# Kernel optimization log

Measured on AMD Instinct MI355X. Metric: run time of the kernel, lower is better.

Reference implementation:

```python
import jax, jax.numpy as jnp
import numpy as np
import math

B, L, D, H, TOPK = 2, 2048, 1024, 16, 5
DK = D // H
U = min(TOPK * int(np.ceil(np.log1p(L))), L)  # = 40 selected queries


def setup_inputs() -> dict:
    k = jax.random.key(0)
    ks = jax.random.split(k, 9)
    s = 1.0 / math.sqrt(D)  # ~ torch Linear init scale
    return {
        "query": jax.random.normal(ks[0], (B, L, D), jnp.float32),
        "key": jax.random.normal(ks[1], (B, L, D), jnp.float32),
        "value": jax.random.normal(ks[2], (B, L, D), jnp.float32),
        "Wq": jax.random.uniform(ks[3], (D, D), jnp.float32, -s, s),
        "bq": jax.random.uniform(ks[4], (D,), jnp.float32, -s, s),
        "Wk": jax.random.uniform(ks[5], (D, D), jnp.float32, -s, s),
        "bk": jax.random.uniform(ks[6], (D,), jnp.float32, -s, s),
        "Wv": jax.random.uniform(ks[7], (D, D), jnp.float32, -s, s),
        "bv": jax.random.uniform(ks[8], (D,), jnp.float32, -s, s),
    }


def reference(query, key, value, Wq, bq, Wk, bk, Wv, bv):
    # torch Linear: y = x @ W.T + b ; split_heads -> [B, H, L, DK]
    def split(x):
        return x.reshape(B, L, H, DK).transpose(0, 2, 1, 3)

    Q = split(query @ Wq.T + bq)
    K = split(key @ Wk.T + bk)
    V = split(value @ Wv.T + bv)

    # Full score matrix [B,H,L,L]; used only for the sparsity measure M
    # (original's Q_K_sample actually uses full K; sampling is dead code).
    scores_full = jnp.einsum('bhqd,bhkd->bhqk', Q, K)
    M = scores_full.max(axis=-1) - scores_full.mean(axis=-1)  # [B,H,L]

    _, M_top = jax.lax.top_k(M, U)  # [B,H,U] (torch uses sorted=False; set identical)

    Q_red = jnp.take_along_axis(Q, M_top[..., None], axis=2)  # [B,H,U,DK]
    attn_scores = jnp.einsum('bhqd,bhkd->bhqk', Q_red, K) / math.sqrt(DK)

    # default causal mask rows gathered at the selected query positions
    causal = jnp.triu(jnp.ones((L, L), jnp.float32), 1)  # [L_Q, L_K]
    attn_scores = attn_scores + causal[M_top] * (-1e9)   # [B,H,U,L]

    attn_probs = jax.nn.softmax(attn_scores, axis=-1)
    attn = jnp.einsum('bhql,bhld->bqhd', attn_probs, V).reshape(B, U, D)
    return attn, attn_probs
```

## Files before the change

### kernel.cpp

```cpp
#include <hip/hip_runtime.h>
#include <hip/hip_bf16.h>

#define BB 2
#define LL 2048
#define DD 1024
#define HH 16
#define DK 64
#define UU 40
#define BH (BB*HH)

typedef unsigned short u16;
typedef float f32x4 __attribute__((ext_vector_type(4)));
typedef short s16x8 __attribute__((ext_vector_type(8)));

__device__ inline float b2f_r8(u16 x) {
    union { unsigned short u; __hip_bfloat16 b; } c; c.u = x;
    return __bfloat162float(c.b);
}
__device__ inline float ldf_r8(const void* p, size_t i, int isF) {
    return isF ? ((const float*)p)[i] : b2f_r8(((const u16*)p)[i]);
}
__device__ inline f32x4 ld4_r8(const void* p, size_t i, int isF) {
    if (isF) return *(const f32x4*)((const float*)p + i);
    ushort4 v = *(const ushort4*)((const u16*)p + i);
    f32x4 r;
    r[0] = b2f_r8(v.x); r[1] = b2f_r8(v.y); r[2] = b2f_r8(v.z); r[3] = b2f_r8(v.w);
    return r;
}
__device__ inline void cvt2_r8(float x, u16& h, u16& l) {
    union { __hip_bfloat16 b; u16 u; } ch, cl;
    ch.b = __float2bfloat16(x);
    float hf = __bfloat162float(ch.b);
    cl.b = __float2bfloat16(x - hf);
    h = ch.u; l = cl.u;
}

__global__ __launch_bounds__(256) void detect_dtype_r8(const u16* __restrict__ q,
                                                       int* __restrict__ flag) {
    __shared__ float red[256];
    int tid = threadIdx.x;
    float mx = 0.f;
    for (int i = tid; i < 4096; i += 256) {
        float v = fabsf(b2f_r8(q[i]));
        if (!(v < 1e30f)) v = 1e38f;
        mx = fmaxf(mx, v);
    }
    red[tid] = mx; __syncthreads();
    for (int s = 128; s > 0; s >>= 1) {
        if (tid < s) red[tid] = fmaxf(red[tid], red[tid + s]);
        __syncthreads();
    }
    if (tid == 0) *flag = (red[0] > 1e20f) ? 1 : 0;
}

#define PAD 132

__global__ __launch_bounds__(256) void proj_f4_r13(
    const void* __restrict__ key, const void* __restrict__ query,
    const void* __restrict__ Wk, const void* __restrict__ Wq,
    const void* __restrict__ bk, const void* __restrict__ bq,
    float* __restrict__ Kf, float* __restrict__ Qf,
    const int* __restrict__ flag)
{
    __shared__ float sX[32 * PAD];
    __shared__ float sW[32 * 68];
    int tid = threadIdx.x;
    int n0 = blockIdx.x * 128, f0 = blockIdx.y * 64, z = blockIdx.z;
    const void* X    = z ? query : key;
    const void* W    = z ? Wq    : Wk;
    const void* bias = z ? bq    : bk;
    float* out       = z ? Qf    : Kf;
    int isF = *flag;
    int tx = tid & 15, ty = tid >> 4;

    float acc[8][4];
#pragma unroll
    for (int a = 0; a < 8; ++a)
#pragma unroll
        for (int c = 0; c < 4; ++c) acc[a][c] = 0.f;

    for (int kc = 0; kc < 32; ++kc) {
        __syncthreads();
#pragma unroll
        for (int it = 0; it < 4; ++it) {
            int row = 64 * (it & 1) + (tid >> 2);
            int d4 = (tid & 3) | ((it >> 1) << 2);
            f32x4 v = ld4_r8(X, (size_t)(n0 + row) * DD + kc * 32 + d4 * 4, isF);
#pragma unroll
            for (int cc = 0; cc < 4; ++cc)
                sX[(4 * d4 + cc) * PAD + row] = v[cc];
        }
#pragma unroll
        for (int it = 0; it < 2; ++it) {
            int row = tid >> 2;
            int d4 = (tid & 3) | (it << 2);
            f32x4 v = ld4_r8(W, (size_t)(f0 + row) * DD + kc * 32 + d4 * 4, isF);
#pragma unroll
            for (int cc = 0; cc < 4; ++cc)
                sW[(4 * d4 + cc) * 68 + row] = v[cc];
        }
        __syncthreads();
        for (int d = 0; d < 32; ++d) {
            const f32x4 xa = *(const f32x4*)(&sX[d * PAD + ty * 4]);
            const f32x4 xb = *(const f32x4*)(&sX[d * PAD + 64 + ty * 4]);
            const f32x4 wa = *(const f32x4*)(&sW[d * 68 + tx * 4]);
            float xv[8] = {xa[0], xa[1], xa[2], xa[3], xb[0], xb[1], xb[2], xb[3]};
#pragma unroll
            for (int a = 0; a < 8; ++a)
#pragma unroll
                for (int c = 0; c < 4; ++c)
                    acc[a][c] = fmaf(xv[a], wa[c], acc[a][c]);
        }
    }
#pragma unroll
    for (int a = 0; a < 8; ++a) {
        int n = n0 + (a >> 2) * 64 + ty * 4 + (a & 3);
        int b = n >> 11, l = n & (LL - 1);
#pragma unroll
        for (int c = 0; c < 4; ++c) {
            int f = f0 + tx * 4 + c;
            int h = f >> 6, dk = f & 63;
            out[((size_t)(b * HH + h) * LL + l) * DK + dk] =
                acc[a][c] + ldf_r8(bias, (size_t)f, isF);
        }
    }
}

__global__ __launch_bounds__(256) void preconvW_r16(
    const void* __restrict__ Wv, u16* __restrict__ Whi, u16* __restrict__ Wlo,
    const int* __restrict__ flag)
{
    int isF = *flag;
    size_t i = ((size_t)blockIdx.x * 256 + threadIdx.x) * 4;
    f32x4 v = ld4_r8(Wv, i, isF);
    ushort4 h4, l4;
    cvt2_r8(v[0], h4.x, l4.x);
    cvt2_r8(v[1], h4.y, l4.y);
    cvt2_r8(v[2], h4.z, l4.z);
    cvt2_r8(v[3], h4.w, l4.w);
    *(ushort4*)&Whi[i] = h4;
    *(ushort4*)&Wlo[i] = l4;
}

#define LDK 72
__global__ __launch_bounds__(256) void proj_mfma_v_r16(
    const void* __restrict__ X, const u16* __restrict__ Whi,
    const u16* __restrict__ Wlo, const void* __restrict__ bias,
    float* __restrict__ out, const int* __restrict__ flag)
{
    __shared__ u16 Ahi[64 * LDK];
    __shared__ u16 Alo[64 * LDK];
    __shared__ u16 Bhi[128 * LDK];
    __shared__ u16 Blo[128 * LDK];
    int tid = threadIdx.x;
    int n0 = blockIdx.x * 64, f0 = blockIdx.y * 128;
    int isF = *flag;
    int lane = tid & 63, w = tid >> 6, wr = w >> 1, wc = w & 1;

    f32x4 acc[2][4] = {};

    for (int kc = 0; kc < 16; ++kc) {
        __syncthreads();
#pragma unroll
        for (int it = 0; it < 4; ++it) {
            int i = it * 256 + tid;
            int row = i >> 4, c = (i & 15) << 2;
            f32x4 v = ld4_r8(X, (size_t)(n0 + row) * DD + kc * 64 + c, isF);
            ushort4 h4, l4;
            cvt2_r8(v[0], h4.x, l4.x);
            cvt2_r8(v[1], h4.y, l4.y);
            cvt2_r8(v[2], h4.z, l4.z);
            cvt2_r8(v[3], h4.w, l4.w);
            *(ushort4*)&Ahi[row * LDK + c] = h4;
            *(ushort4*)&Alo[row * LDK + c] = l4;
        }
#pragma unroll
        for (int it = 0; it < 8; ++it) {
            int i = it * 256 + tid;
            int row = i >> 4, c = (i & 15) << 2;
            size_t go = (size_t)(f0 + row) * DD + kc * 64 + c;
            *(ushort4*)&Bhi[row * LDK + c] = *(const ushort4*)&Whi[go];
            *(ushort4*)&Blo[row * LDK + c] = *(const ushort4*)&Wlo[go];
        }
        __syncthreads();
#pragma unroll
        for (int kk = 0; kk < 2; ++kk) {
            int koff = kk * 32 + (lane >> 4) * 8;
            s16x8 ah[2], al[2];
#pragma unroll
            for (int mi = 0; mi < 2; ++mi) {
                int r = wr * 32 + mi * 16 + (lane & 15);
                ah[mi] = *(const s16x8*)&Ahi[r * LDK + koff];
                al[mi] = *(const s16x8*)&Alo[r * LDK + koff];
            }
#pragma unroll
            for (int ni = 0; ni < 4; ++ni) {
                int r = wc * 64 + ni * 16 + (lane & 15);
                s16x8 bh = *(const s16x8*)&Bhi[r * LDK + koff];
                s16x8 bl = *(const s16x8*)&Blo[r * LDK + koff];
#pragma unroll
                for (int mi = 0; mi < 2; ++mi) {
                    acc[mi][ni] = __builtin_amdgcn_mfma_f32_16x16x32_bf16(ah[mi], bh, acc[mi][ni], 0, 0, 0);
                    acc[mi][ni] = __builtin_amdgcn_mfma_f32_16x16x32_bf16(al[mi], bh, acc[mi][ni], 0, 0, 0);
                    acc[mi][ni] = __builtin_amdgcn_mfma_f32_16x16x32_bf16(ah[mi], bl, acc[mi][ni], 0, 0, 0);
                }
            }
        }
    }

#pragma unroll
    for (int ni = 0; ni < 4; ++ni) {
        int f = f0 + wc * 64 + ni * 16 + (lane & 15);
        float bb = ldf_r8(bias, (size_t)f, isF);
        int h = f >> 6, dk = f & 63;
#pragma unroll
        for (int mi = 0; mi < 2; ++mi) {
            int nbase = n0 + wr * 32 + mi * 16 + ((lane >> 4) << 2);
#pragma unroll
            for (int j2 = 0; j2 < 4; ++j2) {
                int n = nbase + j2, b = n >> 11, l = n & (LL - 1);
                out[((size_t)(b * HH + h) * LL + l) * DK + dk] = acc[mi][ni][j2] + bb;
            }
        }
    }
}

__global__ __launch_bounds__(256) void kbar_r8(
    const float* __restrict__ Kf, double* __restrict__ Kbar)
{
    __shared__ double red[256];
    int bh = blockIdx.x, tid = threadIdx.x;
    int d = tid & 63, seg = tid >> 6;
    double s = 0;
    for (int l = seg * 512; l < seg * 512 + 512; ++l)
        s += (double)Kf[((size_t)bh * LL + l) * DK + d];
    red[tid] = s; __syncthreads();
    if (tid < 128) red[tid] += red[tid + 128];
    __syncthreads();
    if (tid < 64) Kbar[(size_t)bh * DK + d] = (red[tid] + red[tid + 64]) * (1.0 / (double)LL);
}

#define QTS 128
__global__ __launch_bounds__(256) void stats_max_r12(
    const float* __restrict__ Qf, const float* __restrict__ Kf,
    const double* __restrict__ Kbar, double* __restrict__ Mv)
{
    __shared__ float sQ[64 * PAD];
    __shared__ float sK[64 * 68];
    __shared__ float rowmax[QTS];
    int tid = threadIdx.x;
    int q0 = blockIdx.x * QTS, bh = blockIdx.y;
    int tx = tid & 15, ty = tid >> 4;

    {
        const float* src = Qf + ((size_t)bh * LL + q0) * DK;
#pragma unroll
        for (int it = 0; it < 8; ++it) {
            int row = 64 * (it & 1) + (tid >> 2);
            int d4 = (tid & 3) | ((it >> 1) << 2);
            f32x4 v = *(const f32x4*)(src + (size_t)row * DK + d4 * 4);
#pragma unroll
            for (int cc = 0; cc < 4; ++cc)
                sQ[(4 * d4 + cc) * PAD + row] = v[cc];
        }
    }
    float rmax8[8];
#pragma unroll
    for (int a = 0; a < 8; ++a) rmax8[a] = -INFINITY;

    const float* kbase = Kf + (size_t)bh * LL * DK;
    for (int kc = 0; kc < 32; ++kc) {
        __syncthreads();
#pragma unroll
        for (int it = 0; it < 4; ++it) {
            int row = tid >> 2;
            int d4 = (tid & 3) | (it << 2);
            f32x4 v = *(const f32x4*)(kbase + (size_t)(kc * 64 + row) * DK + d4 * 4);
#pragma unroll
            for (int cc = 0; cc < 4; ++cc)
                sK[(4 * d4 + cc) * 68 + row] = v[cc];
        }
        __syncthreads();
        float acc[8][4];
#pragma unroll
        for (int a = 0; a < 8; ++a)
#pragma unroll
            for (int c = 0; c < 4; ++c) acc[a][c] = 0.f;
        for (int d = 0; d < 64; ++d) {
            const f32x4 qa = *(const f32x4*)(&sQ[d * PAD + ty * 4]);
            const f32x4 qb = *(const f32x4*)(&sQ[d * PAD + 64 + ty * 4]);
            const f32x4 ka = *(const f32x4*)(&sK[d * 68 + tx * 4]);
            float qv[8] = {qa[0], qa[1], qa[2], qa[3], qb[0], qb[1], qb[2], qb[3]};
#pragma unroll
            for (int a = 0; a < 8; ++a)
#pragma unroll
                for (int c = 0; c < 4; ++c)
                    acc[a][c] = fmaf(qv[a], ka[c], acc[a][c]);
        }
#pragma unroll
        for (int a = 0; a < 8; ++a)
#pragma unroll
            for (int c = 0; c < 4; ++c) rmax8[a] = fmaxf(rmax8[a], acc[a][c]);
    }
#pragma unroll
    for (int a = 0; a < 8; ++a) {
        float v = rmax8[a];
        v = fmaxf(v, __shfl_xor(v, 1));
        v = fmaxf(v, __shfl_xor(v, 2));
        v = fmaxf(v, __shfl_xor(v, 4));
        v = fmaxf(v, __shfl_xor(v, 8));
        rmax8[a] = v;
    }
    if (tx == 0) {
#pragma unroll
        for (int a = 0; a < 8; ++a) {
            int row = ty * 4 + (a & 3) + (a >> 2) * 64;
            rowmax[row] = rmax8[a];
        }
    }
    __syncthreads();
    if (tid < QTS) {
        const double* kb = Kbar + (size_t)bh * DK;
        double s = 0;
#pragma unroll
        for (int d = 0; d < 64; ++d) s += (double)sQ[d * PAD + tid] * kb[d];
        Mv[(size_t)bh * LL + q0 + tid] = (double)rowmax[tid] - s;
    }
}

__global__ __launch_bounds__(64) void topk_wave_r10(
    const double* __restrict__ Mv, int* __restrict__ sel)
{
    int bh = blockIdx.x, lane = threadIdx.x;
    double v[32];
#pragma unroll
    for (int t = 0; t < 32; ++t) v[t] = Mv[(size_t)bh * LL + t * 64 + lane];
    for (int u = 0; u < UU; ++u) {
        double bv = -1e301; int bi = LL;
#pragma unroll
        for (int t = 0; t < 32; ++t) {
            double x = v[t]; int j = t * 64 + lane;
            if (x > bv || (x == bv && j < bi)) { bv = x; bi = j; }
        }
#pragma unroll
        for (int off = 1; off < 64; off <<= 1) {
            double ov = __shfl_xor(bv, off); int oi = __shfl_xor(bi, off);
            if (ov > bv || (ov == bv && oi < bi)) { bv = ov; bi = oi; }
        }
        if ((bi & 63) == lane) {
            int ts = bi >> 6;
#pragma unroll
            for (int t = 0; t < 32; ++t)
                if (t == ts) v[t] = -1e302;
        }
        if (lane == 0) sel[bh * UU + u] = bi;
    }
}

__global__ __launch_bounds__(256) void scores_r15(
    const float* __restrict__ Qf, const float* __restrict__ Kf,
    const int* __restrict__ sel, float* __restrict__ S)
{
    __shared__ float sK[128 * 68];
    __shared__ float qsm[40 * 68];
    __shared__ int qpos[UU];
    int lq = blockIdx.x, bh = blockIdx.y, tid = threadIdx.x;
    int l0 = lq * 128;
    if (tid < UU) qpos[tid] = sel[bh * UU + tid];
    __syncthreads();
    for (int i = tid; i < 640; i += 256) {
        int u = i >> 4, c4 = i & 15;
        *(f32x4*)&qsm[u * 68 + c4 * 4] =
            *(const f32x4*)&Qf[((size_t)bh * LL + qpos[u]) * DK + c4 * 4];
    }
#pragma unroll
    for (int it = 0; it < 8; ++it) {
        int idx = it * 256 + tid;
        int l = idx >> 4, d4 = idx & 15;
        *(f32x4*)&sK[l * 68 + d4 * 4] =
            *(const f32x4*)&Kf[((size_t)bh * LL + l0 + l) * DK + d4 * 4];
    }
    __syncthreads();
    int gu = tid >> 5, lt = tid & 31;
    float acc[5][4];
#pragma unroll
    for (int ui = 0; ui < 5; ++ui)
#pragma unroll
        for (int li = 0; li < 4; ++li) acc[ui][li] = 0.f;
    for (int d16 = 0; d16 < 16; ++d16) {
        f32x4 qf[5], kf[4];
#pragma unroll
        for (int ui = 0; ui < 5; ++ui)
            qf[ui] = *(const f32x4*)&qsm[(gu + 8 * ui) * 68 + d16 * 4];
#pragma unroll
        for (int li = 0; li < 4; ++li)
            kf[li] = *(const f32x4*)&sK[(lt + 32 * li) * 68 + d16 * 4];
#pragma unroll
        for (int ui = 0; ui < 5; ++ui)
#pragma unroll
            for (int li = 0; li < 4; ++li)
#pragma unroll
                for (int c = 0; c < 4; ++c)
                    acc[ui][li] = fmaf(qf[ui][c], kf[li][c], acc[ui][li]);
    }
#pragma unroll
    for (int ui = 0; ui < 5; ++ui) {
        int u = gu + 8 * ui;
        int qp = qpos[u];
#pragma unroll
        for (int li = 0; li < 4; ++li) {
            int l = l0 + lt + 32 * li;
            float s = acc[ui][li] * 0.125f;
            if (l > qp) s -= 1e9f;
            S[((size_t)bh * UU + u) * LL + l] = s;
        }
    }
}

__global__ __launch_bounds__(256) void softmax_r12(
    const float* __restrict__ S, float* __restrict__ probsOut)
{
    __shared__ float red[256];
    int u = blockIdx.x, bh = blockIdx.y, tid = threadIdx.x;
    size_t rowo = ((size_t)bh * UU + u) * LL;
    float sloc[8];
    float lmax = -INFINITY;
#pragma unroll
    for (int c = 0; c < 8; ++c) {
        sloc[c] = S[rowo + c * 256 + tid];
        lmax = fmaxf(lmax, sloc[c]);
    }
    red[tid] = lmax; __syncthreads();
    for (int s2 = 128; s2 > 0; s2 >>= 1) {
        if (tid < s2) red[tid] = fmaxf(red[tid], red[tid + s2]);
        __syncthreads();
    }
    float mval = red[0];
    __syncthreads();
    float lsum = 0.f;
#pragma unroll
    for (int c = 0; c < 8; ++c) { sloc[c] = expf(sloc[c] - mval); lsum += sloc[c]; }
    red[tid] = lsum; __syncthreads();
    for (int s2 = 128; s2 > 0; s2 >>= 1) {
        if (tid < s2) red[tid] += red[tid + s2];
        __syncthreads();
    }
    float inv = 1.0f / red[0];
#pragma unroll
    for (int c = 0; c < 8; ++c)
        probsOut[rowo + c * 256 + tid] = sloc[c] * inv;
}

__global__ __launch_bounds__(256) void pv_r15(
    const float* __restrict__ probsOut, const float* __restrict__ Vf,
    float* __restrict__ part)
{
    __shared__ float pP[20 * 256];
    int lq = blockIdx.x, bh = blockIdx.y, ug2 = blockIdx.z, tid = threadIdx.x;
    int l0 = lq * 256;
#pragma unroll
    for (int it = 0; it < 5; ++it) {
        int idx = it * 256 + tid;
        int ur = idx >> 6, l4 = idx & 63;
        *(f32x4*)&pP[ur * 256 + l4 * 4] =
            *(const f32x4*)&probsOut[((size_t)bh * UU + ug2 * 20 + ur) * LL + l0 + l4 * 4];
    }
    __syncthreads();
    int dk = tid & 63, ug = tid >> 6;
    const float* vb = Vf + ((size_t)bh * LL + l0) * DK + dk;
    float acc[5];
#pragma unroll
    for (int j = 0; j < 5; ++j) acc[j] = 0.f;
    for (int l4 = 0; l4 < 64; ++l4) {
        float vv0 = vb[(size_t)(l4 * 4 + 0) * DK];
        float vv1 = vb[(size_t)(l4 * 4 + 1) * DK];
        float vv2 = vb[(size_t)(l4 * 4 + 2) * DK];
        float vv3 = vb[(size_t)(l4 * 4 + 3) * DK];
#pragma unroll
        for (int j = 0; j < 5; ++j) {
            const f32x4 p4 = *(const f32x4*)&pP[(ug * 5 + j) * 256 + l4 * 4];
            acc[j] = fmaf(p4[0], vv0, acc[j]);
            acc[j] = fmaf(p4[1], vv1, acc[j]);
            acc[j] = fmaf(p4[2], vv2, acc[j]);
            acc[j] = fmaf(p4[3], vv3, acc[j]);
        }
    }
#pragma unroll
    for (int j = 0; j < 5; ++j) {
        int u = ug2 * 20 + ug * 5 + j;
        part[(((size_t)bh * 8 + lq) * UU + u) * DK + dk] = acc[j];
    }
}

__global__ __launch_bounds__(64) void pvred_r12(
    const float* __restrict__ part, float* __restrict__ attnOut)
{
    int u = blockIdx.x, bh = blockIdx.y, dk = threadIdx.x;
    int b = bh >> 4, h = bh & 15;
    float s = 0.f;
#pragma unroll
    for (int lq = 0; lq < 8; ++lq)
        s += part[(((size_t)bh * 8 + lq) * UU + u) * DK + dk];
    attnOut[((size_t)b * UU + u) * DD + h * DK + dk] = s;
}

extern "C" void kernel_launch(void* const* d_in, const int* in_sizes, int n_in,
                              void* d_out, int out_size, void* d_ws, size_t ws_size,
                              hipStream_t stream) {
    (void)in_sizes; (void)n_in; (void)out_size; (void)ws_size;
    const void* query = d_in[0];
    const void* key   = d_in[1];
    const void* value = d_in[2];
    const void* Wq    = d_in[3];
    const void* bq    = d_in[4];
    const void* Wk    = d_in[5];
    const void* bk    = d_in[6];
    const void* Wv    = d_in[7];
    const void* bv    = d_in[8];

    char* w = (char*)d_ws;
    const size_t NE = (size_t)BB * HH * LL * DK;
    float* Kf  = (float*)w;  w += NE * 4;
    float* Vf  = (float*)w;  w += NE * 4;
    float* Qf  = (float*)w;  w += NE * 4;
    double* Mv = (double*)w; w += (size_t)BH * LL * 8;
    double* Kbar = (double*)w; w += (size_t)BH * DK * 8;
    int* sel   = (int*)w;    w += (size_t)BH * UU * 4;
    int* flag  = (int*)w;    w += 64;
    float* S    = (float*)w; w += (size_t)BH * UU * LL * 4;
    float* part = (float*)w; w += (size_t)BH * 8 * UU * DK * 4;
    u16* Whi = (u16*)w;      w += (size_t)DD * DD * 2;
    u16* Wlo = (u16*)w;      w += (size_t)DD * DD * 2;

    float* attnOut  = (float*)d_out;
    float* probsOut = attnOut + (size_t)BB * UU * DD;

    dim3 blk(256);
    detect_dtype_r8<<<1, blk, 0, stream>>>((const u16*)query, flag);
    preconvW_r16<<<1024, blk, 0, stream>>>(Wv, Whi, Wlo, flag);
    proj_f4_r13<<<dim3(32, 16, 2), blk, 0, stream>>>(key, query, Wk, Wq, bk, bq,
                                                     Kf, Qf, flag);
    proj_mfma_v_r16<<<dim3(64, 8), blk, 0, stream>>>(value, Whi, Wlo, bv, Vf, flag);
    kbar_r8<<<32, blk, 0, stream>>>(Kf, Kbar);
    stats_max_r12<<<dim3(LL / QTS, 32), blk, 0, stream>>>(Qf, Kf, Kbar, Mv);
    topk_wave_r10<<<32, dim3(64), 0, stream>>>(Mv, sel);
    scores_r15<<<dim3(16, 32), blk, 0, stream>>>(Qf, Kf, sel, S);
    softmax_r12<<<dim3(UU, 32), blk, 0, stream>>>(S, probsOut);
    pv_r15<<<dim3(8, 32, 2), blk, 0, stream>>>(probsOut, Vf, part);
    pvred_r12<<<dim3(UU, 32), dim3(64), 0, stream>>>(part, attnOut);
}
```

Before: 821.1 us.

## Compute row-max stats with split-bf16 MFMA plus exact fp32 rescue of ambiguous rows

Replaces the fp32 FMA row-max score kernel with a bf16 hi/lo split MFMA kernel that tracks top-2 scores and the argmax per query row. A rescue kernel recomputes the argmax score exactly in fp32 and computes the mean term in double. Rows whose top-2 gap falls below a threshold go on an atomic list, and a follow-up kernel recomputes them with a full fp32 scan. This moves the dominant QK^T max onto matrix cores while keeping exactness where it matters, at the cost of two extra launches and an atomic counter reset in the dtype kernel.

```diff
diff --git a/kernel.cpp b/kernel.cpp
--- a/kernel.cpp
+++ b/kernel.cpp
@@ -35,8 +35,9 @@
     h = ch.u; l = cl.u;
 }
 
-__global__ __launch_bounds__(256) void detect_dtype_r8(const u16* __restrict__ q,
-                                                       int* __restrict__ flag) {
+__global__ __launch_bounds__(256) void detect_dtype_r17(const u16* __restrict__ q,
+                                                        int* __restrict__ flag,
+                                                        int* __restrict__ cnt) {
     __shared__ float red[256];
     int tid = threadIdx.x;
     float mx = 0.f;
@@ -50,7 +51,7 @@
         if (tid < s) red[tid] = fmaxf(red[tid], red[tid + s]);
         __syncthreads();
     }
-    if (tid == 0) *flag = (red[0] > 1e20f) ? 1 : 0;
+    if (tid == 0) { *flag = (red[0] > 1e20f) ? 1 : 0; *cnt = 0; }
 }
 
 #define PAD 132
@@ -240,91 +241,187 @@
     if (tid < 64) Kbar[(size_t)bh * DK + d] = (red[tid] + red[tid + 64]) * (1.0 / (double)LL);
 }
 
-#define QTS 128
-__global__ __launch_bounds__(256) void stats_max_r12(
+__global__ __launch_bounds__(256) void statsq_r17(
     const float* __restrict__ Qf, const float* __restrict__ Kf,
-    const double* __restrict__ Kbar, double* __restrict__ Mv)
-{
-    __shared__ float sQ[64 * PAD];
-    __shared__ float sK[64 * 68];
-    __shared__ float rowmax[QTS];
+    float* __restrict__ M1, int* __restrict__ I1, float* __restrict__ M2)
+{
+    __shared__ u16 Qhi[128 * LDK];
+    __shared__ u16 Qlo[128 * LDK];
+    __shared__ u16 Khi[128 * LDK];
+    __shared__ u16 Klo[128 * LDK];
     int tid = threadIdx.x;
-    int q0 = blockIdx.x * QTS, bh = blockIdx.y;
-    int tx = tid & 15, ty = tid >> 4;
-
-    {
-        const float* src = Qf + ((size_t)bh * LL + q0) * DK;
+    int q0 = blockIdx.x * 128, bh = blockIdx.y;
+    int lane = tid & 63, w = tid >> 6;
+    int qw = w * 32;
+
+#pragma unroll
+    for (int it = 0; it < 8; ++it) {
+        int i = it * 256 + tid;
+        int row = i >> 4, c = (i & 15) << 2;
+        f32x4 v = *(const f32x4*)&Qf[((size_t)bh * LL + q0 + row) * DK + c];
+        ushort4 h4, l4;
+        cvt2_r8(v[0], h4.x, l4.x);
+        cvt2_r8(v[1], h4.y, l4.y);
+        cvt2_r8(v[2], h4.z, l4.z);
+        cvt2_r8(v[3], h4.w, l4.w);
+        *(ushort4*)&Qhi[row * LDK + c] = h4;
+        *(ushort4*)&Qlo[row * LDK + c] = l4;
+    }
+    __syncthreads();
+    s16x8 Bh[2][2], Bl[2][2];
+#pragma unroll
+    for (int qi = 0; qi < 2; ++qi)
+#pragma unroll
+        for (int kk = 0; kk < 2; ++kk) {
+            int r = qw + qi * 16 + (lane & 15);
+            int koff = kk * 32 + (lane >> 4) * 8;
+            Bh[qi][kk] = *(const s16x8*)&Qhi[r * LDK + koff];
+            Bl[qi][kk] = *(const s16x8*)&Qlo[r * LDK + koff];
+        }
+
+    float m1[2] = {-1e30f, -1e30f}, m2[2] = {-1e30f, -1e30f};
+    int i1[2] = {0, 0};
+
+    for (int kt = 0; kt < 16; ++kt) {
+        __syncthreads();
+        int kbase = kt * 128;
 #pragma unroll
         for (int it = 0; it < 8; ++it) {
-            int row = 64 * (it & 1) + (tid >> 2);
-            int d4 = (tid & 3) | ((it >> 1) << 2);
-            f32x4 v = *(const f32x4*)(src + (size_t)row * DK + d4 * 4);
-#pragma unroll
-            for (int cc = 0; cc < 4; ++cc)
-                sQ[(4 * d4 + cc) * PAD + row] = v[cc];
-        }
-    }
-    float rmax8[8];
-#pragma unroll
-    for (int a = 0; a < 8; ++a) rmax8[a] = -INFINITY;
-
-    const float* kbase = Kf + (size_t)bh * LL * DK;
-    for (int kc = 0; kc < 32; ++kc) {
-        __syncthreads();
-#pragma unroll
-        for (int it = 0; it < 4; ++it) {
-            int row = tid >> 2;
-            int d4 = (tid & 3) | (it << 2);
-            f32x4 v = *(const f32x4*)(kbase + (size_t)(kc * 64 + row) * DK + d4 * 4);
-#pragma unroll
-            for (int cc = 0; cc < 4; ++cc)
-                sK[(4 * d4 + cc) * 68 + row] = v[cc];
-        }
-        __syncthreads();
-        float acc[8][4];
-#pragma unroll
-        for (int a = 0; a < 8; ++a)
-#pragma unroll
-            for (int c = 0; c < 4; ++c) acc[a][c] = 0.f;
-        for (int d = 0; d < 64; ++d) {
-            const f32x4 qa = *(const f32x4*)(&sQ[d * PAD + ty * 4]);
-            const f32x4 qb = *(const f32x4*)(&sQ[d * PAD + 64 + ty * 4]);
-            const f32x4 ka = *(const f32x4*)(&sK[d * 68 + tx * 4]);
-            float qv[8] = {qa[0], qa[1], qa[2], qa[3], qb[0], qb[1], qb[2], qb[3]};
-#pragma unroll
-            for (int a = 0; a < 8; ++a)
-#pragma unroll
-                for (int c = 0; c < 4; ++c)
-                    acc[a][c] = fmaf(qv[a], ka[c], acc[a][c]);
-        }
-#pragma unroll
-        for (int a = 0; a < 8; ++a)
-#pragma unroll
-            for (int c = 0; c < 4; ++c) rmax8[a] = fmaxf(rmax8[a], acc[a][c]);
-    }
-#pragma unroll
-    for (int a = 0; a < 8; ++a) {
-        float v = rmax8[a];
-        v = fmaxf(v, __shfl_xor(v, 1));
-        v = fmaxf(v, __shfl_xor(v, 2));
-        v = fmaxf(v, __shfl_xor(v, 4));
-        v = fmaxf(v, __shfl_xor(v, 8));
-        rmax8[a] = v;
-    }
-    if (tx == 0) {
-#pragma unroll
-        for (int a = 0; a < 8; ++a) {
-            int row = ty * 4 + (a & 3) + (a >> 2) * 64;
-            rowmax[row] = rmax8[a];
-        }
-    }
-    __syncthreads();
-    if (tid < QTS) {
-        const double* kb = Kbar + (size_t)bh * DK;
-        double s = 0;
-#pragma unroll
-        for (int d = 0; d < 64; ++d) s += (double)sQ[d * PAD + tid] * kb[d];
-        Mv[(size_t)bh * LL + q0 + tid] = (double)rowmax[tid] - s;
+            int i = it * 256 + tid;
+            int row = i >> 4, c = (i & 15) << 2;
+            f32x4 v = *(const f32x4*)&Kf[((size_t)bh * LL + kbase + row) * DK + c];
+            ushort4 h4, l4;
+            cvt2_r8(v[0], h4.x, l4.x);
+            cvt2_r8(v[1], h4.y, l4.y);
+            cvt2_r8(v[2], h4.z, l4.z);
+            cvt2_r8(v[3], h4.w, l4.w);
+            *(ushort4*)&Khi[row * LDK + c] = h4;
+            *(ushort4*)&Klo[row * LDK + c] = l4;
+        }
+        __syncthreads();
+#pragma unroll
+        for (int ki = 0; ki < 8; ++ki) {
+#pragma unroll
+            for (int qi = 0; qi < 2; ++qi) {
+                f32x4 acc = {0.f, 0.f, 0.f, 0.f};
+#pragma unroll
+                for (int kk = 0; kk < 2; ++kk) {
+                    int koff = kk * 32 + (lane >> 4) * 8;
+                    int r = ki * 16 + (lane & 15);
+                    s16x8 Ah = *(const s16x8*)&Khi[r * LDK + koff];
+                    s16x8 Al = *(const s16x8*)&Klo[r * LDK + koff];
+                    acc = __builtin_amdgcn_mfma_f32_16x16x32_bf16(Ah, Bh[qi][kk], acc, 0, 0, 0);
+                    acc = __builtin_amdgcn_mfma_f32_16x16x32_bf16(Al, Bh[qi][kk], acc, 0, 0, 0);
+                    acc = __builtin_amdgcn_mfma_f32_16x16x32_bf16(Ah, Bl[qi][kk], acc, 0, 0, 0);
+                }
+#pragma unroll
+                for (int j = 0; j < 4; ++j) {
+                    float val = acc[j];
+                    int kg = kbase + ki * 16 + ((lane >> 4) << 2) + j;
+                    bool g1 = val > m1[qi];
+                    bool g2 = val > m2[qi];
+                    m2[qi] = g1 ? m1[qi] : (g2 ? val : m2[qi]);
+                    i1[qi] = g1 ? kg : i1[qi];
+                    m1[qi] = g1 ? val : m1[qi];
+                }
+            }
+        }
+    }
+#pragma unroll
+    for (int qi = 0; qi < 2; ++qi) {
+#pragma unroll
+        for (int off = 16; off <= 32; off <<= 1) {
+            float ov1 = __shfl_xor(m1[qi], off);
+            int oi1 = __shfl_xor(i1[qi], off);
+            float ov2 = __shfl_xor(m2[qi], off);
+            if (ov1 > m1[qi]) {
+                m2[qi] = fmaxf(m1[qi], ov2);
+                m1[qi] = ov1; i1[qi] = oi1;
+            } else {
+                m2[qi] = fmaxf(m2[qi], fmaxf(ov1, ov2) == ov1 ? ov1 : ov2);
+                m2[qi] = fmaxf(m2[qi], ov1);
+            }
+        }
+    }
+    if ((lane >> 4) == 0) {
+#pragma unroll
+        for (int qi = 0; qi < 2; ++qi) {
+            int q = q0 + qw + qi * 16 + (lane & 15);
+            size_t o = (size_t)bh * LL + q;
+            M1[o] = m1[qi]; I1[o] = i1[qi]; M2[o] = m2[qi];
+        }
+    }
+}
+
+#define GAPTHR 0.02f
+__global__ __launch_bounds__(256) void rescue_r17(
+    const float* __restrict__ Qf, const float* __restrict__ Kf,
+    const double* __restrict__ Kbar, const float* __restrict__ M1,
+    const int* __restrict__ I1, const float* __restrict__ M2,
+    double* __restrict__ Mv, int* __restrict__ alist, int* __restrict__ cnt)
+{
+    int gid = blockIdx.x * 256 + threadIdx.x;
+    int bh = gid >> 11, q = gid & (LL - 1);
+    const float* qp = Qf + ((size_t)bh * LL + q) * DK;
+    const float* kp = Kf + ((size_t)bh * LL + I1[gid]) * DK;
+    float s = 0.f;
+    for (int d4 = 0; d4 < 16; ++d4) {
+        const f32x4 qv = *(const f32x4*)(qp + d4 * 4);
+        const f32x4 kv = *(const f32x4*)(kp + d4 * 4);
+        s = fmaf(qv[0], kv[0], s);
+        s = fmaf(qv[1], kv[1], s);
+        s = fmaf(qv[2], kv[2], s);
+        s = fmaf(qv[3], kv[3], s);
+    }
+    const double* kb = Kbar + (size_t)bh * DK;
+    double md = 0;
+    for (int d = 0; d < DK; ++d) md += (double)qp[d] * kb[d];
+    Mv[gid] = (double)s - md;
+    if (!(M1[gid] - M2[gid] > GAPTHR)) {
+        int slot = atomicAdd(cnt, 1);
+        alist[slot] = gid;
+    }
+}
+
+__global__ __launch_bounds__(256) void ambig_r17(
+    const float* __restrict__ Qf, const float* __restrict__ Kf,
+    const double* __restrict__ Kbar, const int* __restrict__ alist,
+    const int* __restrict__ cnt, double* __restrict__ Mv)
+{
+    int lane = threadIdx.x & 63;
+    int wid = blockIdx.x * 4 + (threadIdx.x >> 6);
+    int n = *cnt;
+    for (int sIdx = wid; sIdx < n; sIdx += 512) {
+        int gid = alist[sIdx];
+        int bh = gid >> 11, q = gid & (LL - 1);
+        const float* qp = Qf + ((size_t)bh * LL + q) * DK;
+        f32x4 qr[16];
+#pragma unroll
+        for (int d4 = 0; d4 < 16; ++d4) qr[d4] = *(const f32x4*)(qp + d4 * 4);
+        float mx = -1e30f;
+        for (int t = 0; t < 32; ++t) {
+            int k = t * 64 + lane;
+            const float* kp = Kf + ((size_t)bh * LL + k) * DK;
+            float s = 0.f;
+#pragma unroll
+            for (int d4 = 0; d4 < 16; ++d4) {
+                const f32x4 kv = *(const f32x4*)(kp + d4 * 4);
+                s = fmaf(qr[d4][0], kv[0], s);
+                s = fmaf(qr[d4][1], kv[1], s);
+                s = fmaf(qr[d4][2], kv[2], s);
+                s = fmaf(qr[d4][3], kv[3], s);
+            }
+            mx = fmaxf(mx, s);
+        }
+#pragma unroll
+        for (int off = 1; off < 64; off <<= 1)
+            mx = fmaxf(mx, __shfl_xor(mx, off));
+        if (lane == 0) {
+            const double* kb = Kbar + (size_t)bh * DK;
+            double md = 0;
+            for (int d = 0; d < DK; ++d) md += (double)qp[d] * kb[d];
+            Mv[gid] = (double)mx - md;
+        }
     }
 }
 
@@ -531,18 +628,25 @@
     float* part = (float*)w; w += (size_t)BH * 8 * UU * DK * 4;
     u16* Whi = (u16*)w;      w += (size_t)DD * DD * 2;
     u16* Wlo = (u16*)w;      w += (size_t)DD * DD * 2;
+    float* M1 = (float*)w;   w += (size_t)BH * LL * 4;
+    float* M2 = (float*)w;   w += (size_t)BH * LL * 4;
+    int* I1   = (int*)w;     w += (size_t)BH * LL * 4;
+    int* alist = (int*)w;    w += (size_t)BH * LL * 4;
+    int* cnt  = (int*)w;     w += 64;
 
     float* attnOut  = (float*)d_out;
     float* probsOut = attnOut + (size_t)BB * UU * DD;
 
     dim3 blk(256);
-    detect_dtype_r8<<<1, blk, 0, stream>>>((const u16*)query, flag);
+    detect_dtype_r17<<<1, blk, 0, stream>>>((const u16*)query, flag, cnt);
     preconvW_r16<<<1024, blk, 0, stream>>>(Wv, Whi, Wlo, flag);
     proj_f4_r13<<<dim3(32, 16, 2), blk, 0, stream>>>(key, query, Wk, Wq, bk, bq,
                                                      Kf, Qf, flag);
     proj_mfma_v_r16<<<dim3(64, 8), blk, 0, stream>>>(value, Whi, Wlo, bv, Vf, flag);
     kbar_r8<<<32, blk, 0, stream>>>(Kf, Kbar);
-    stats_max_r12<<<dim3(LL / QTS, 32), blk, 0, stream>>>(Qf, Kf, Kbar, Mv);
+    statsq_r17<<<dim3(16, 32), blk, 0, stream>>>(Qf, Kf, M1, I1, M2);
+    rescue_r17<<<256, blk, 0, stream>>>(Qf, Kf, Kbar, M1, I1, M2, Mv, alist, cnt);
+    ambig_r17<<<128, blk, 0, stream>>>(Qf, Kf, Kbar, alist, cnt, Mv);
     topk_wave_r10<<<32, dim3(64), 0, stream>>>(Mv, sel);
     scores_r15<<<dim3(16, 32), blk, 0, stream>>>(Qf, Kf, sel, S);
     softmax_r12<<<dim3(UU, 32), blk, 0, stream>>>(S, probsOut);
```

Result: slower. 932.4 us (+13.6%).
